# Optimization experiments

Measured on AMD Instinct MI355X. Metric: run time of the kernel, lower is better.

Reference implementation:

```python
import jax, jax.numpy as jnp
import numpy as np

N, E, D, H, L, T = 50000, 200000, 128, 64, 2, 4
SIB_ID = 1
EPS = 1e-6


def _log_map_zero(x, c):
    # x: [N, D+1] on hyperboloid of curvature c; returns [N, D] tangent at origin.
    sqrt_c = jnp.sqrt(c)
    x0 = jnp.clip(sqrt_c * x[..., 0], 1.0 + 1e-7, None)
    dist = jnp.arccosh(x0) / sqrt_c                      # [N]
    sp = x[..., 1:]                                      # [N, D]
    nrm = jnp.maximum(jnp.linalg.norm(sp, axis=-1), EPS)
    return sp * (dist / nrm)[..., None]


def _exp_map_zero(v, c):
    # v: [N, D] tangent at origin; returns [N, D+1] on hyperboloid.
    sqrt_c = jnp.sqrt(c)
    nrm = jnp.maximum(jnp.linalg.norm(v, axis=-1), EPS)  # [N]
    th = sqrt_c * nrm
    x0 = jnp.cosh(th) / sqrt_c
    sp = v * (jnp.sinh(th) / (sqrt_c * nrm))[..., None]
    return jnp.concatenate([x0[..., None], sp], axis=-1)


def setup_inputs() -> dict:
    key = jax.random.key(0)
    ks = jax.random.split(key, 12)
    v0 = 0.1 * jax.random.normal(ks[0], (N, D), dtype=jnp.float32)
    x_hyp = _exp_map_zero(v0, 1.0)
    edge_index = jax.random.randint(ks[1], (2, E), 0, N, dtype=jnp.int32)
    edge_types = jax.random.randint(ks[2], (E,), 0, T, dtype=jnp.int32)
    edge_weights = jax.random.uniform(ks[3], (E,), dtype=jnp.float32) + 0.1
    s_lin = 1.0 / np.sqrt(D)
    s_w1 = 1.0 / np.sqrt(3 * D)
    s_w2 = 1.0 / np.sqrt(H)
    return {
        "x_hyp": x_hyp,
        "edge_index": edge_index,
        "edge_types": edge_types,
        "edge_weights": edge_weights,
        "lin_w": s_lin * jax.random.normal(ks[4], (L, D, D), dtype=jnp.float32),
        "lin_b": jnp.zeros((L, D), dtype=jnp.float32),
        "ln_g": jnp.ones((L, D), dtype=jnp.float32),
        "ln_b": jnp.zeros((L, D), dtype=jnp.float32),
        "edge_emb": 0.02 * jax.random.normal(ks[5], (L, T, D), dtype=jnp.float32),
        "attn_w1": s_w1 * jax.random.normal(ks[6], (L, 3 * D, H), dtype=jnp.float32),
        "attn_b1": jnp.zeros((L, H), dtype=jnp.float32),
        "attn_w2": s_w2 * jax.random.normal(ks[7], (L, H, 1), dtype=jnp.float32),
        "attn_b2": jnp.zeros((L, 1), dtype=jnp.float32),
        "sibling_boost": jnp.full((L,), 0.15, dtype=jnp.float32),
        "curvature": jnp.ones((L,), dtype=jnp.float32),
    }


def _layer(x_hyp, edge_index, edge_types, edge_weights,
           lin_w, lin_b, ln_g, ln_b, emb, w1, b1, w2, b2, sib, curv):
    n = x_hyp.shape[0]
    # curvature is read via .item() in the original -> detached constant
    c = jax.lax.stop_gradient(jnp.clip(curv, 0.1, 10.0))
    x_tan = _log_map_zero(x_hyp, c)                      # [N, D]
    x_lin = x_tan @ lin_w.T + lin_b                      # [N, D]
    src, dst = edge_index[0], edge_index[1]              # PyG: x_j=src, x_i=dst
    x_i = x_lin[dst]                                     # [E, D]
    x_j = x_lin[src]                                     # [E, D]
    e_emb = emb[edge_types]                              # [E, D]
    attn_in = jnp.concatenate([x_i, x_j, e_emb], axis=-1)  # [E, 3D]
    h = jax.nn.silu(attn_in @ w1 + b1)                   # [E, H]
    score = (h @ w2 + b2)[..., 0]                        # [E]
    score = score + jnp.log(jnp.clip(edge_weights, EPS, None))
    score = score + (edge_types == SIB_ID).astype(score.dtype) * sib
    # segment softmax over destination nodes
    seg_max = jax.ops.segment_max(score, dst, num_segments=n)
    ex = jnp.exp(score - seg_max[dst])
    seg_sum = jax.ops.segment_sum(ex, dst, num_segments=n)
    alpha = ex / (seg_sum[dst] + 1e-16)                  # [E]
    msg = (x_j + e_emb) * (alpha * edge_weights)[:, None]  # [E, D]
    x_agg = jax.ops.segment_sum(msg, dst, num_segments=n)  # [N, D]
    x_out = x_tan + x_agg                                # dropout is identity in eval
    mu = jnp.mean(x_out, axis=-1, keepdims=True)
    var = jnp.var(x_out, axis=-1, keepdims=True)
    x_out = (x_out - mu) * jax.lax.rsqrt(var + 1e-5) * ln_g + ln_b
    return _exp_map_zero(x_out, c)


def reference(x_hyp, edge_index, edge_types, edge_weights, lin_w, lin_b,
              ln_g, ln_b, edge_emb, attn_w1, attn_b1, attn_w2, attn_b2,
              sibling_boost, curvature):
    for i in range(lin_w.shape[0]):
        x_hyp = _layer(x_hyp, edge_index, edge_types, edge_weights,
                       lin_w[i], lin_b[i], ln_g[i], ln_b[i], edge_emb[i],
                       attn_w1[i], attn_b1[i], attn_w2[i], attn_b2[i],
                       sibling_boost[i], curvature[i])
    return x_hyp
```

## Files before the change

kernel.cpp:

```cpp
#include <hip/hip_runtime.h>
#include <math.h>

#define WAVE 64
#define KMAX 32

typedef __attribute__((ext_vector_type(8))) short bf16x8;
typedef __attribute__((ext_vector_type(4))) float f32x4;

__device__ __forceinline__ unsigned short f2b(float f) {
    unsigned u = __float_as_uint(f);
    unsigned r = (u + 0x7FFFu + ((u >> 16) & 1u)) >> 16;
    return (unsigned short)r;
}
__device__ __forceinline__ float b2f(unsigned short u) {
    return __uint_as_float(((unsigned)u) << 16);
}
__device__ __forceinline__ float frcp(float x)   { return __builtin_amdgcn_rcpf(x); }
__device__ __forceinline__ float frsq(float x)   { return __builtin_amdgcn_rsqf(x); }
__device__ __forceinline__ float fsqrt2(float x) { return __builtin_amdgcn_sqrtf(x); }
__device__ __forceinline__ float silu(float x)   { return x * frcp(1.f + __expf(-x)); }
__device__ __forceinline__ float facosh(float x) { return __logf(x + fsqrt2(x * x - 1.f)); }

__device__ __forceinline__ void dual_gemm_16(
    unsigned short* sm,
    const unsigned short* __restrict__ LW, const unsigned short* __restrict__ WT,
    const float* __restrict__ bias,
    unsigned short* __restrict__ xlin, unsigned short* __restrict__ acat,
    int base, int N, int tid)
{
    int wave = tid >> 6;
    int lane = tid & 63;
    int quad = lane >> 4;
    int l16  = lane & 15;
    int nloc = tid >> 4;

    __syncthreads();

    bf16x8 a[4];
    #pragma unroll
    for (int kk = 0; kk < 4; ++kk)
        a[kk] = *(const bf16x8*)&sm[l16 * 136 + kk * 32 + quad * 8];

    f32x4 acc[2];
    acc[0] = (f32x4){0.f, 0.f, 0.f, 0.f};
    acc[1] = (f32x4){0.f, 0.f, 0.f, 0.f};
    #pragma unroll
    for (int kk = 0; kk < 4; ++kk) {
        #pragma unroll
        for (int t = 0; t < 2; ++t) {
            int nt = wave * 2 + t;
            bf16x8 b = *(const bf16x8*)&LW[(size_t)(nt * 16 + l16) * 128 + kk * 32 + quad * 8];
            acc[t] = __builtin_amdgcn_mfma_f32_16x16x32_bf16(a[kk], b, acc[t], 0, 0, 0);
        }
    }
    __syncthreads();
    #pragma unroll
    for (int t = 0; t < 2; ++t) {
        int nt = wave * 2 + t;
        float bv = bias[nt * 16 + l16];
        #pragma unroll
        for (int r = 0; r < 4; ++r)
            sm[(quad * 4 + r) * 136 + nt * 16 + l16] = f2b(acc[t][r] + bv);
    }
    __syncthreads();

    bf16x8 a2[4];
    #pragma unroll
    for (int kk = 0; kk < 4; ++kk)
        a2[kk] = *(const bf16x8*)&sm[l16 * 136 + kk * 32 + quad * 8];
    int node = base + nloc;
    if (node < N)
        *(bf16x8*)&xlin[(size_t)node * 128 + 8 * l16] =
            *(const bf16x8*)&sm[nloc * 136 + 8 * l16];

    f32x4 acc2[2];
    acc2[0] = (f32x4){0.f, 0.f, 0.f, 0.f};
    acc2[1] = (f32x4){0.f, 0.f, 0.f, 0.f};
    #pragma unroll
    for (int kk = 0; kk < 4; ++kk) {
        #pragma unroll
        for (int t = 0; t < 2; ++t) {
            int nt = wave * 2 + t;
            bf16x8 b = *(const bf16x8*)&WT[(size_t)(nt * 16 + l16) * 128 + kk * 32 + quad * 8];
            acc2[t] = __builtin_amdgcn_mfma_f32_16x16x32_bf16(a2[kk], b, acc2[t], 0, 0, 0);
        }
    }
    #pragma unroll
    for (int t = 0; t < 2; ++t) {
        int nt = wave * 2 + t;
        #pragma unroll
        for (int r = 0; r < 4; ++r) {
            int rr = base + quad * 4 + r;
            if (rr < N) acat[(size_t)rr * 128 + nt * 16 + l16] = f2b(acc2[t][r]);
        }
    }
}

__global__ __launch_bounds__(256) void k_pre(
    const float* __restrict__ lin_w, const float* __restrict__ w1,
    const float* __restrict__ b1, const float* __restrict__ emb,
    unsigned short* __restrict__ lw_bf, unsigned short* __restrict__ Wt_bf,
    float* __restrict__ ae, int* __restrict__ deg, int N, int PB)
{
    int bid = blockIdx.x, tid = threadIdx.x;
    if (bid < PB) {
        int l = bid / 129, bx = bid % 129;
        const float* lwl = lin_w + (size_t)l * 16384;
        const float* w1l = w1 + (size_t)l * 384 * 64;
        if (bx < 64) {
            int idx = bx * 256 + tid;
            lw_bf[l * 16384 + idx] = f2b(lwl[idx]);
        } else if (bx < 128) {
            int idx = (bx - 64) * 256 + tid;
            int o = idx >> 7, i = idx & 127;
            float v = (o < 64) ? w1l[i * 64 + o] : w1l[(128 + i) * 64 + (o - 64)];
            Wt_bf[l * 16384 + idx] = f2b(v);
        } else {
            int t = tid >> 6, h = tid & 63;
            float s = b1[l * 64 + h];
            #pragma unroll 8
            for (int i = 0; i < 128; ++i)
                s += emb[l * 512 + t * 128 + i] * w1l[(256 + i) * 64 + h];
            ae[l * 256 + tid] = s;
        }
    } else {
        int i0 = ((bid - PB) * 256 + tid) * 4;
        if (i0 + 3 < N) {
            *(int4*)&deg[i0] = make_int4(0, 0, 0, 0);
        } else {
            #pragma unroll
            for (int k2 = 0; k2 < 4; ++k2)
                if (i0 + k2 < N) deg[i0 + k2] = 0;
        }
    }
}

__global__ __launch_bounds__(256) void k_main(
    const int* __restrict__ ei, const int* __restrict__ et,
    const float* __restrict__ ew, const float* __restrict__ xh,
    const float* __restrict__ curv,
    const unsigned short* __restrict__ LW, const unsigned short* __restrict__ WT,
    const float* __restrict__ lb,
    int* __restrict__ deg, int2* __restrict__ epack,
    unsigned short* __restrict__ xtan_bf,
    unsigned short* __restrict__ xlin, unsigned short* __restrict__ acat,
    int E, int N, int ECH)
{
    __shared__ __align__(16) unsigned short sm[16 * 136];
    int bid = blockIdx.x, tid = threadIdx.x;
    if (bid < ECH) {
        int e = bid * 256 + tid;
        if (e < E) {
            int dst = ei[E + e];
            int rank = atomicAdd(&deg[dst], 1);
            if (rank < KMAX) {
                int2 r;
                r.x = ei[e] | (et[e] << 24);
                r.y = __float_as_int(ew[e]);
                epack[(size_t)dst * KMAX + rank] = r;
            }
        }
        return;
    }
    int base = (bid - ECH) * 16;
    int l16  = tid & 15;
    int nloc = tid >> 4;
    int node = base + nloc;
    int nodec = node < N ? node : N - 1;

    float c = fminf(fmaxf(curv[0], 0.1f), 10.f);
    float sqc = fsqrt2(c);
    const float* row = xh + (size_t)nodec * 129;
    float x0 = row[0];
    float v[8];
    #pragma unroll
    for (int j = 0; j < 8; ++j) v[j] = row[1 + 8 * l16 + j];
    float n2 = 0.f;
    #pragma unroll
    for (int j = 0; j < 8; ++j) n2 += v[j] * v[j];
    #pragma unroll
    for (int m = 1; m < 16; m <<= 1) n2 += __shfl_xor(n2, m, WAVE);
    float nrm = fmaxf(fsqrt2(n2), 1e-6f);
    float x0c = fmaxf(sqc * x0, 1.f + 1e-7f);
    float f = facosh(x0c) * frcp(sqc) * frcp(nrm);

    bf16x8 o8;
    #pragma unroll
    for (int j = 0; j < 8; ++j) o8[j] = (short)f2b(v[j] * f);
    if (node < N)
        *(bf16x8*)&xtan_bf[(size_t)node * 128 + 8 * l16] = o8;
    *(bf16x8*)&sm[nloc * 136 + 8 * l16] = o8;

    dual_gemm_16(sm, LW, WT, lb, xlin, acat, base, N, tid);
}

__global__ __launch_bounds__(256) void k_B(
    const int* __restrict__ deg, const int2* __restrict__ epack,
    const unsigned short* __restrict__ acat, const unsigned short* __restrict__ xlin,
    unsigned short* __restrict__ xtan_bf, const float* __restrict__ ae,
    const float* __restrict__ emb, const float* __restrict__ w2,
    const float* __restrict__ b2, const float* __restrict__ sib,
    const float* __restrict__ g, const float* __restrict__ b,
    const float* __restrict__ curv, const float* __restrict__ curv_n,
    int last, float* __restrict__ out, int N,
    const unsigned short* __restrict__ LWn, const unsigned short* __restrict__ WTn,
    const float* __restrict__ lbn,
    unsigned short* __restrict__ xlin_o, unsigned short* __restrict__ acat_o)
{
    __shared__ __align__(16) unsigned short sm[16 * 136];
    int tid = threadIdx.x;
    int lane = tid & 63;
    int quad = lane >> 4;
    int l16  = lane & 15;
    int gw = (blockIdx.x * 256 + tid) >> 6;
    int wid = gw * 4 + quad;
    bool nv = wid < N;
    int widc = nv ? wid : N - 1;

    int dg = deg[widc];
    const int4* bp = (const int4*)(epack + widc * KMAX);
    int4 myent = bp[l16];
    bf16x8 xtu = *(const bf16x8*)&xtan_bf[(size_t)widc * 128 + 8 * l16];
    ushort4 adu = *(const ushort4*)&acat[(size_t)widc * 128 + 4 * l16];
    float4 w2v = *(const float4*)&w2[4 * l16];

    float c = fminf(fmaxf(curv[0], 0.1f), 10.f);
    float sqc = fsqrt2(c);
    float rsqc = frcp(sqc);
    dg = dg < KMAX ? dg : KMAX;
    dg = nv ? dg : 0;

    float ad0 = b2f(adu.x), ad1 = b2f(adu.y), ad2 = b2f(adu.z), ad3 = b2f(adu.w);
    float b2v = b2[0], sibv = sib[0];

    float acc[8];
    #pragma unroll
    for (int j = 0; j < 8; ++j) acc[j] = 0.f;
    float S = 0.f;
    float4 St = make_float4(0.f, 0.f, 0.f, 0.f);

    int jmax = dg;
    jmax = max(jmax, __shfl_xor(jmax, 16, WAVE));
    jmax = max(jmax, __shfl_xor(jmax, 32, WAVE));

    ushort4 asu_n; bf16x8 xu_n; float4 av_n;
    float w_n = 1.f; int t_n = 0; bool ev_n = false;

#define FETCH(J) {                                                          \
        int lsrc = (quad << 4) + ((J) >> 1);                                \
        int rx = __shfl(((J) & 1) ? myent.z : myent.x, lsrc, WAVE);         \
        int ry = __shfl(((J) & 1) ? myent.w : myent.y, lsrc, WAVE);         \
        ev_n = (J) < dg;                                                    \
        int src = ev_n ? (rx & 0xFFFFFF) : 0;                               \
        t_n = ev_n ? (int)(((unsigned)rx) >> 24) : 0;                       \
        float wv = __int_as_float(ry);                                      \
        w_n = ev_n ? wv : 1.f;                                              \
        asu_n = *(const ushort4*)&acat[(size_t)src * 128 + 64 + 4 * l16];   \
        av_n  = *(const float4*)&ae[t_n * 64 + 4 * l16];                    \
        xu_n  = *(const bf16x8*)&xlin[(size_t)src * 128 + 8 * l16];         \
    }

    if (jmax > 0) FETCH(0);
    for (int j = 0; j < jmax; ++j) {
        ushort4 asu = asu_n; bf16x8 xu = xu_n; float4 av = av_n;
        float w = w_n; int t = t_n; bool ev = ev_n;
        if (j + 1 < jmax) FETCH(j + 1);

        float d = silu(ad0 + b2f(asu.x) + av.x) * w2v.x
                + silu(ad1 + b2f(asu.y) + av.y) * w2v.y
                + silu(ad2 + b2f(asu.z) + av.z) * w2v.z
                + silu(ad3 + b2f(asu.w) + av.w) * w2v.w;
        #pragma unroll
        for (int m = 1; m < 16; m <<= 1) d += __shfl_xor(d, m, WAVE);
        float s = d + b2v + __logf(fmaxf(w, 1e-6f));
        if (t == 1) s += sibv;
        float exv = ev ? __expf(s) : 0.f;
        S += exv;
        float cf = exv * w;

        #pragma unroll
        for (int k = 0; k < 8; ++k)
            acc[k] += b2f((unsigned short)xu[k]) * cf;
        St.x += (t == 0) ? cf : 0.f;
        St.y += (t == 1) ? cf : 0.f;
        St.z += (t == 2) ? cf : 0.f;
        St.w += (t == 3) ? cf : 0.f;
    }
#undef FETCH

    #pragma unroll
    for (int tt = 0; tt < 4; ++tt) {
        float stv = (tt == 0) ? St.x : (tt == 1) ? St.y : (tt == 2) ? St.z : St.w;
        float4 em0 = *(const float4*)&emb[tt * 128 + 8 * l16];
        float4 em1 = *(const float4*)&emb[tt * 128 + 8 * l16 + 4];
        acc[0] += em0.x * stv; acc[1] += em0.y * stv;
        acc[2] += em0.z * stv; acc[3] += em0.w * stv;
        acc[4] += em1.x * stv; acc[5] += em1.y * stv;
        acc[6] += em1.z * stv; acc[7] += em1.w * stv;
    }

    float inv = frcp(S + 1e-16f);
    float y[8];
    #pragma unroll
    for (int j = 0; j < 8; ++j)
        y[j] = b2f((unsigned short)xtu[j]) + acc[j] * inv;

    float sum = 0.f, sq = 0.f;
    #pragma unroll
    for (int j = 0; j < 8; ++j) { sum += y[j]; sq += y[j] * y[j]; }
    #pragma unroll
    for (int m = 1; m < 16; m <<= 1) {
        sum += __shfl_xor(sum, m, WAVE);
        sq  += __shfl_xor(sq, m, WAVE);
    }
    float mu = sum * (1.f / 128.f);
    float var = sq * (1.f / 128.f) - mu * mu;
    float invs = frsq(var + 1e-5f);
    float4 g0 = *(const float4*)&g[8 * l16];
    float4 g1 = *(const float4*)&g[8 * l16 + 4];
    float4 bb0 = *(const float4*)&b[8 * l16];
    float4 bb1 = *(const float4*)&b[8 * l16 + 4];
    y[0] = (y[0] - mu) * invs * g0.x + bb0.x;
    y[1] = (y[1] - mu) * invs * g0.y + bb0.y;
    y[2] = (y[2] - mu) * invs * g0.z + bb0.z;
    y[3] = (y[3] - mu) * invs * g0.w + bb0.w;
    y[4] = (y[4] - mu) * invs * g1.x + bb1.x;
    y[5] = (y[5] - mu) * invs * g1.y + bb1.y;
    y[6] = (y[6] - mu) * invs * g1.z + bb1.z;
    y[7] = (y[7] - mu) * invs * g1.w + bb1.w;

    float nrm2 = 0.f;
    #pragma unroll
    for (int j = 0; j < 8; ++j) nrm2 += y[j] * y[j];
    #pragma unroll
    for (int m = 1; m < 16; m <<= 1) nrm2 += __shfl_xor(nrm2, m, WAVE);
    float nrm = fmaxf(fsqrt2(nrm2), 1e-6f);
    float th = sqc * nrm;
    float e = __expf(th);
    float einv = frcp(e);
    float ch = 0.5f * (e + einv);
    float sh = 0.5f * (e - einv);
    float sc = sh * frcp(sqc * nrm);

    if (last) {
        if (nv) {
            float* o = out + (size_t)wid * 129;
            if (l16 == 0) o[0] = ch * rsqc;
            #pragma unroll
            for (int j = 0; j < 8; ++j) o[1 + 8 * l16 + j] = y[j] * sc;
        }
    } else {
        float x0 = ch * rsqc;
        float c2 = fminf(fmaxf(curv_n[0], 0.1f), 10.f);
        float sqc2 = fsqrt2(c2);
        float x0c = fmaxf(sqc2 * x0, 1.f + 1e-7f);
        float dist = facosh(x0c) * frcp(sqc2);
        float nsp = fmaxf(sh * rsqc, 1e-6f);
        float sf = sc * dist * frcp(nsp);
        bf16x8 o8;
        #pragma unroll
        for (int j = 0; j < 8; ++j) o8[j] = (short)f2b(y[j] * sf);
        if (nv)
            *(bf16x8*)&xtan_bf[(size_t)wid * 128 + 8 * l16] = o8;
        *(bf16x8*)&sm[(tid >> 4) * 136 + 8 * l16] = o8;
        dual_gemm_16(sm, LWn, WTn, lbn, xlin_o, acat_o, blockIdx.x * 16, N, tid);
    }
}

extern "C" void kernel_launch(void* const* d_in, const int* in_sizes, int n_in,
                              void* d_out, int out_size, void* d_ws, size_t ws_size,
                              hipStream_t stream) {
    const float* x_hyp = (const float*)d_in[0];
    const int*   ei    = (const int*)d_in[1];
    const int*   et    = (const int*)d_in[2];
    const float* ew    = (const float*)d_in[3];
    const float* lin_w = (const float*)d_in[4];
    const float* lin_b = (const float*)d_in[5];
    const float* ln_g  = (const float*)d_in[6];
    const float* ln_b  = (const float*)d_in[7];
    const float* emb   = (const float*)d_in[8];
    const float* w1    = (const float*)d_in[9];
    const float* b1    = (const float*)d_in[10];
    const float* w2    = (const float*)d_in[11];
    const float* b2    = (const float*)d_in[12];
    const float* sib   = (const float*)d_in[13];
    const float* curv  = (const float*)d_in[14];
    float* out = (float*)d_out;

    const int N = in_sizes[0] / 129;
    const int E = in_sizes[2];
    const int L = in_sizes[4] / (128 * 128);
    const int ECH = (E + 255) / 256;
    const int NB16 = (N + 15) / 16;
    const int PB = L * 129;
    const int ZB = (N + 1023) / 1024;

    unsigned short* xtan_bf = (unsigned short*)d_ws;
    unsigned short* xlin0 = xtan_bf + (size_t)N * 128;
    unsigned short* acat0 = xlin0 + (size_t)N * 128;
    unsigned short* xlin1 = acat0 + (size_t)N * 128;
    unsigned short* acat1 = xlin1 + (size_t)N * 128;
    int2* epack = (int2*)(acat1 + (size_t)N * 128);
    unsigned short* lw_bf = (unsigned short*)(epack + (size_t)N * KMAX);
    unsigned short* Wt_bf = lw_bf + (size_t)L * 16384;
    float* ae   = (float*)(Wt_bf + (size_t)L * 16384);
    int* deg    = (int*)(ae + (size_t)L * 256);

    k_pre<<<PB + ZB, 256, 0, stream>>>(lin_w, w1, b1, emb,
                                       lw_bf, Wt_bf, ae, deg, N, PB);

    k_main<<<ECH + NB16, 256, 0, stream>>>(
        ei, et, ew, x_hyp, curv, lw_bf, Wt_bf, lin_b,
        deg, epack, xtan_bf, xlin0, acat0, E, N, ECH);

    for (int l = 0; l < L; ++l) {
        int ln = (l + 1 < L) ? l + 1 : l;
        unsigned short* xin = (l & 1) ? xlin1 : xlin0;
        unsigned short* ain = (l & 1) ? acat1 : acat0;
        unsigned short* xot = (l & 1) ? xlin0 : xlin1;
        unsigned short* aot = (l & 1) ? acat0 : acat1;
        k_B<<<NB16, 256, 0, stream>>>(
            deg, epack, ain, xin, xtan_bf,
            ae + (size_t)l * 256, emb + (size_t)l * 512,
            w2 + (size_t)l * 64, b2 + l, sib + l,
            ln_g + (size_t)l * 128, ln_b + (size_t)l * 128,
            curv + l, curv + ln,
            l == L - 1 ? 1 : 0, out, N,
            lw_bf + (size_t)ln * 16384, Wt_bf + (size_t)ln * 16384,
            lin_b + (size_t)ln * 128, xot, aot);
    }
}
```

Baseline: 222.8 us.

## Assign one wave per node in k_B, splitting edges across quads

After: 324.2 us. 1.46x slower.

```diff
diff --git a/kernel.cpp b/kernel.cpp
--- a/kernel.cpp
+++ b/kernel.cpp
@@ -194,7 +194,7 @@
     dual_gemm_16(sm, LW, WT, lb, xlin, acat, base, N, tid);
 }
 
-__global__ __launch_bounds__(256) void k_B(
+__global__ __launch_bounds__(1024, 8) void k_B(
     const int* __restrict__ deg, const int2* __restrict__ epack,
     const unsigned short* __restrict__ acat, const unsigned short* __restrict__ xlin,
     unsigned short* __restrict__ xtan_bf, const float* __restrict__ ae,
@@ -208,18 +208,18 @@
     unsigned short* __restrict__ xlin_o, unsigned short* __restrict__ acat_o)
 {
     __shared__ __align__(16) unsigned short sm[16 * 136];
-    int tid = threadIdx.x;
+    int tid  = threadIdx.x;
+    int wv   = tid >> 6;
     int lane = tid & 63;
     int quad = lane >> 4;
     int l16  = lane & 15;
-    int gw = (blockIdx.x * 256 + tid) >> 6;
-    int wid = gw * 4 + quad;
-    bool nv = wid < N;
+    int base = blockIdx.x * 16;
+    int wid  = base + wv;
+    bool nv  = wid < N;
     int widc = nv ? wid : N - 1;
 
     int dg = deg[widc];
-    const int4* bp = (const int4*)(epack + widc * KMAX);
-    int4 myent = bp[l16];
+    int2 my2 = epack[(size_t)widc * KMAX + (lane & 31)];
     bf16x8 xtu = *(const bf16x8*)&xtan_bf[(size_t)widc * 128 + 8 * l16];
     ushort4 adu = *(const ushort4*)&acat[(size_t)widc * 128 + 4 * l16];
     float4 w2v = *(const float4*)&w2[4 * l16];
@@ -229,6 +229,7 @@
     float rsqc = frcp(sqc);
     dg = dg < KMAX ? dg : KMAX;
     dg = nv ? dg : 0;
+    int jmax = (dg + 3) >> 2;
 
     float ad0 = b2f(adu.x), ad1 = b2f(adu.y), ad2 = b2f(adu.z), ad3 = b2f(adu.w);
     float b2v = b2[0], sibv = sib[0];
@@ -239,22 +240,18 @@
     float S = 0.f;
     float4 St = make_float4(0.f, 0.f, 0.f, 0.f);
 
-    int jmax = dg;
-    jmax = max(jmax, __shfl_xor(jmax, 16, WAVE));
-    jmax = max(jmax, __shfl_xor(jmax, 32, WAVE));
-
     ushort4 asu_n; bf16x8 xu_n; float4 av_n;
     float w_n = 1.f; int t_n = 0; bool ev_n = false;
 
 #define FETCH(J) {                                                          \
-        int lsrc = (quad << 4) + ((J) >> 1);                                \
-        int rx = __shfl(((J) & 1) ? myent.z : myent.x, lsrc, WAVE);         \
-        int ry = __shfl(((J) & 1) ? myent.w : myent.y, lsrc, WAVE);         \
-        ev_n = (J) < dg;                                                    \
+        int eidx = (J) * 4 + quad;                                          \
+        int rx = __shfl(my2.x, eidx, WAVE);                                 \
+        int ry = __shfl(my2.y, eidx, WAVE);                                 \
+        ev_n = eidx < dg;                                                   \
         int src = ev_n ? (rx & 0xFFFFFF) : 0;                               \
         t_n = ev_n ? (int)(((unsigned)rx) >> 24) : 0;                       \
-        float wv = __int_as_float(ry);                                      \
-        w_n = ev_n ? wv : 1.f;                                              \
+        float wv_ = __int_as_float(ry);                                     \
+        w_n = ev_n ? wv_ : 1.f;                                             \
         asu_n = *(const ushort4*)&acat[(size_t)src * 128 + 64 + 4 * l16];   \
         av_n  = *(const float4*)&ae[t_n * 64 + 4 * l16];                    \
         xu_n  = *(const bf16x8*)&xlin[(size_t)src * 128 + 8 * l16];         \
@@ -287,6 +284,17 @@
         St.w += (t == 3) ? cf : 0.f;
     }
 #undef FETCH
+
+    #pragma unroll
+    for (int k = 0; k < 8; ++k) {
+        acc[k] += __shfl_xor(acc[k], 16, WAVE);
+        acc[k] += __shfl_xor(acc[k], 32, WAVE);
+    }
+    S += __shfl_xor(S, 16, WAVE);  S += __shfl_xor(S, 32, WAVE);
+    St.x += __shfl_xor(St.x, 16, WAVE); St.x += __shfl_xor(St.x, 32, WAVE);
+    St.y += __shfl_xor(St.y, 16, WAVE); St.y += __shfl_xor(St.y, 32, WAVE);
+    St.z += __shfl_xor(St.z, 16, WAVE); St.z += __shfl_xor(St.z, 32, WAVE);
+    St.w += __shfl_xor(St.w, 16, WAVE); St.w += __shfl_xor(St.w, 32, WAVE);
 
     #pragma unroll
     for (int tt = 0; tt < 4; ++tt) {
@@ -343,27 +351,77 @@
     float sc = sh * frcp(sqc * nrm);
 
     if (last) {
-        if (nv) {
+        if (nv && quad == 0) {
             float* o = out + (size_t)wid * 129;
             if (l16 == 0) o[0] = ch * rsqc;
             #pragma unroll
             for (int j = 0; j < 8; ++j) o[1 + 8 * l16 + j] = y[j] * sc;
         }
-    } else {
-        float x0 = ch * rsqc;
-        float c2 = fminf(fmaxf(curv_n[0], 0.1f), 10.f);
-        float sqc2 = fsqrt2(c2);
-        float x0c = fmaxf(sqc2 * x0, 1.f + 1e-7f);
-        float dist = facosh(x0c) * frcp(sqc2);
-        float nsp = fmaxf(sh * rsqc, 1e-6f);
-        float sf = sc * dist * frcp(nsp);
-        bf16x8 o8;
-        #pragma unroll
-        for (int j = 0; j < 8; ++j) o8[j] = (short)f2b(y[j] * sf);
-        if (nv)
-            *(bf16x8*)&xtan_bf[(size_t)wid * 128 + 8 * l16] = o8;
-        *(bf16x8*)&sm[(tid >> 4) * 136 + 8 * l16] = o8;
-        dual_gemm_16(sm, LWn, WTn, lbn, xlin_o, acat_o, blockIdx.x * 16, N, tid);
+        return;
+    }
+
+    float x0 = ch * rsqc;
+    float c2 = fminf(fmaxf(curv_n[0], 0.1f), 10.f);
+    float sqc2 = fsqrt2(c2);
+    float x0c = fmaxf(sqc2 * x0, 1.f + 1e-7f);
+    float dist = facosh(x0c) * frcp(sqc2);
+    float nsp = fmaxf(sh * rsqc, 1e-6f);
+    float sf = sc * dist * frcp(nsp);
+    bf16x8 o8;
+    #pragma unroll
+    for (int j = 0; j < 8; ++j) o8[j] = (short)f2b(y[j] * sf);
+    if (quad == 0) {
+        if (nv) *(bf16x8*)&xtan_bf[(size_t)wid * 128 + 8 * l16] = o8;
+        *(bf16x8*)&sm[wv * 136 + 8 * l16] = o8;
+    }
+
+    __syncthreads();
+    bf16x8 a[4];
+    if (wv < 8) {
+        #pragma unroll
+        for (int kk = 0; kk < 4; ++kk)
+            a[kk] = *(const bf16x8*)&sm[l16 * 136 + kk * 32 + quad * 8];
+    }
+    f32x4 acc1 = (f32x4){0.f, 0.f, 0.f, 0.f};
+    if (wv < 8) {
+        #pragma unroll
+        for (int kk = 0; kk < 4; ++kk) {
+            bf16x8 bb = *(const bf16x8*)&LWn[(size_t)(wv * 16 + l16) * 128 + kk * 32 + quad * 8];
+            acc1 = __builtin_amdgcn_mfma_f32_16x16x32_bf16(a[kk], bb, acc1, 0, 0, 0);
+        }
+    }
+    __syncthreads();
+    if (wv < 8) {
+        float bv = lbn[wv * 16 + l16];
+        #pragma unroll
+        for (int r = 0; r < 4; ++r)
+            sm[(quad * 4 + r) * 136 + wv * 16 + l16] = f2b(acc1[r] + bv);
+    }
+    __syncthreads();
+
+    if (tid < 256) {
+        int node2 = base + (tid >> 4);
+        if (node2 < N)
+            *(bf16x8*)&xlin_o[(size_t)node2 * 128 + 8 * (tid & 15)] =
+                *(const bf16x8*)&sm[(tid >> 4) * 136 + 8 * (tid & 15)];
+    }
+    if (wv >= 8) {
+        int ct = wv - 8;
+        bf16x8 a2[4];
+        #pragma unroll
+        for (int kk = 0; kk < 4; ++kk)
+            a2[kk] = *(const bf16x8*)&sm[l16 * 136 + kk * 32 + quad * 8];
+        f32x4 acc2 = (f32x4){0.f, 0.f, 0.f, 0.f};
+        #pragma unroll
+        for (int kk = 0; kk < 4; ++kk) {
+            bf16x8 bb = *(const bf16x8*)&WTn[(size_t)(ct * 16 + l16) * 128 + kk * 32 + quad * 8];
+            acc2 = __builtin_amdgcn_mfma_f32_16x16x32_bf16(a2[kk], bb, acc2, 0, 0, 0);
+        }
+        #pragma unroll
+        for (int r = 0; r < 4; ++r) {
+            int rr = base + quad * 4 + r;
+            if (rr < N) acat_o[(size_t)rr * 128 + ct * 16 + l16] = f2b(acc2[r]);
+        }
     }
 }
 
@@ -419,7 +477,7 @@
         unsigned short* ain = (l & 1) ? acat1 : acat0;
         unsigned short* xot = (l & 1) ? xlin0 : xlin1;
         unsigned short* aot = (l & 1) ? acat0 : acat1;
-        k_B<<<NB16, 256, 0, stream>>>(
+        k_B<<<NB16, 1024, 0, stream>>>(
             deg, epack, ain, xin, xtan_bf,
             ae + (size_t)l * 256, emb + (size_t)l * 512,
             w2 + (size_t)l * 64, b2 + l, sib + l,
```
